# Kernel optimization log

Hardware: AMD Instinct MI355X
Metric: run time of the kernel (lower is better)

## Reference

```python
import jax, jax.numpy as jnp
import numpy as np

N_NODES = 50000
N_EDGES = 800000
IN_FEATS = 128
SAGE_HID = 512
H_FEATS = 128
MLP_HID = 32
N_PARTS = 8


def setup_inputs() -> dict:
    key = jax.random.key(0)
    ks = jax.random.split(key, 16)
    s = 0.05
    return {
        "features": jax.random.normal(ks[0], (N_NODES, IN_FEATS), jnp.float32),
        "src": jax.random.randint(ks[1], (N_EDGES,), 0, N_NODES),
        "dst": jax.random.randint(ks[2], (N_EDGES,), 0, N_NODES),
        # SAGEConv layer 1 (in_feats -> 512): fc_self has bias, fc_neigh no bias
        "W1_self": jax.random.normal(ks[3], (IN_FEATS, SAGE_HID), jnp.float32) * s,
        "W1_neigh": jax.random.normal(ks[4], (IN_FEATS, SAGE_HID), jnp.float32) * s,
        "b1": jnp.zeros((SAGE_HID,), jnp.float32),
        # SAGEConv layer 2 (512 -> h_feats)
        "W2_self": jax.random.normal(ks[5], (SAGE_HID, H_FEATS), jnp.float32) * s,
        "W2_neigh": jax.random.normal(ks[6], (SAGE_HID, H_FEATS), jnp.float32) * s,
        "b2": jnp.zeros((H_FEATS,), jnp.float32),
        # Partitioning MLP
        "Wp1": jax.random.normal(ks[7], (H_FEATS, MLP_HID), jnp.float32) * s,
        "bp1": jnp.zeros((MLP_HID,), jnp.float32),
        "Wp2": jax.random.normal(ks[8], (MLP_HID, N_PARTS), jnp.float32) * s,
        "bp2": jnp.zeros((N_PARTS,), jnp.float32),
    }


def _sage_mean(x, src, dst, deg_inv, W_self, W_neigh, b):
    # gather source-node features per edge, sum by destination, divide by in-degree
    agg = jax.ops.segment_sum(jnp.take(x, src, axis=0), dst, num_segments=N_NODES)
    agg = agg * deg_inv[:, None]
    return x @ W_self + agg @ W_neigh + b


def reference(features, src, dst, W1_self, W1_neigh, b1, W2_self, W2_neigh, b2,
              Wp1, bp1, Wp2, bp2):
    deg = jax.ops.segment_sum(jnp.ones_like(dst, dtype=features.dtype), dst,
                              num_segments=N_NODES)
    deg_inv = 1.0 / jnp.maximum(deg, 1.0)
    h = jax.nn.relu(_sage_mean(features, src, dst, deg_inv, W1_self, W1_neigh, b1))
    h = jax.nn.relu(_sage_mean(h, src, dst, deg_inv, W2_self, W2_neigh, b2))
    x = jax.nn.relu(h @ Wp1 + bp1)
    logits = x @ Wp2 + bp2
    return jax.nn.softmax(logits, axis=1)
```

## Files before the change

kernel.cpp:

```cpp
#include <hip/hip_runtime.h>
#include <hip/hip_bf16.h>

#define N_NODES 50000
#define N_EDGES 800000
#define ZROW    N_NODES
#define PADCAP  (N_EDGES + 8 * N_NODES + 64)
#define NCLS    8
#define CLSW    6250

typedef short  short8  __attribute__((ext_vector_type(8)));
typedef float  floatx4 __attribute__((ext_vector_type(4)));

__device__ __forceinline__ short f2bf(float f) {
    union { __hip_bfloat16 h; short s; } u;
    u.h = __float2bfloat16(f);
    return u.s;
}
__device__ __forceinline__ unsigned packbf(float lo, float hi) {
    return ((unsigned)(unsigned short)f2bf(hi) << 16) | (unsigned short)f2bf(lo);
}

__device__ __forceinline__ void acc2(unsigned v, float& ax, float& ay,
                                     unsigned selLo, unsigned selHi) {
    asm("v_dot2_f32_bf16 %0, %1, %2, %0" : "+v"(ax) : "v"(v), "v"(selLo));
    asm("v_dot2_f32_bf16 %0, %1, %2, %0" : "+v"(ay) : "v"(v), "v"(selHi));
}

__device__ __forceinline__ void gld_lds16(const short* g, short* l) {
    __builtin_amdgcn_global_load_lds(
        (const __attribute__((address_space(1))) int*)g,
        (__attribute__((address_space(3))) int*)l, 16, 0, 0);
}

__global__ void k_init(int* __restrict__ deg, int* __restrict__ col,
                       int* __restrict__ zrowA, int* __restrict__ zrowY) {
    int i = blockIdx.x * 256 + threadIdx.x;
    if (i < PADCAP) col[i] = ZROW;
    if (i < N_NODES) deg[i] = 0;
    if (i < 128) zrowA[i] = 0;
    if (i < 64)  zrowY[i] = 0;
}

__global__ void k_deg(const int* __restrict__ dst, int* __restrict__ deg) {
    int e = blockIdx.x * 256 + threadIdx.x;
    if (e < N_EDGES) atomicAdd(&deg[dst[e]], 1);
}

__global__ __launch_bounds__(1024) void k_scan1(const int* __restrict__ deg,
                                                int* __restrict__ bsum,
                                                float* __restrict__ dinv) {
    __shared__ int ws[16];
    int b = blockIdx.x, t = threadIdx.x, i = b * 1024 + t;
    int lane = t & 63, wid = t >> 6;
    int v = (i < N_NODES) ? deg[i] : 0;
    if (i < N_NODES) dinv[i] = 1.0f / fmaxf((float)v, 1.0f);
    int x = (v + 7) & ~7;
    #pragma unroll
    for (int off = 1; off < 64; off <<= 1) x += __shfl_xor(x, off, 64);
    if (lane == 0) ws[wid] = x;
    __syncthreads();
    if (t == 0) {
        int s = 0;
        #pragma unroll
        for (int k = 0; k < 16; ++k) s += ws[k];
        bsum[b] = s;
    }
}

__global__ void k_scan2(const int* __restrict__ bsum, int* __restrict__ boff) {
    int lane = threadIdx.x;
    int v = (lane < 49) ? bsum[lane] : 0;
    int x = v;
    #pragma unroll
    for (int off = 1; off < 64; off <<= 1) {
        int y = __shfl_up(x, off, 64);
        if (lane >= off) x += y;
    }
    if (lane < 49) boff[lane] = x - v;
}

__global__ __launch_bounds__(1024) void k_scan3(const int* __restrict__ deg,
                                                const int* __restrict__ boff,
                                                int* __restrict__ rowptr,
                                                int* __restrict__ cursor) {
    __shared__ int ws[16];
    int b = blockIdx.x, t = threadIdx.x, i = b * 1024 + t;
    int lane = t & 63, wid = t >> 6;
    int v = (i < N_NODES) ? ((deg[i] + 7) & ~7) : 0;
    int x = v;
    #pragma unroll
    for (int off = 1; off < 64; off <<= 1) {
        int y = __shfl_up(x, off, 64);
        if (lane >= off) x += y;
    }
    if (lane == 63) ws[wid] = x;
    __syncthreads();
    if (wid == 0) {
        int s = (lane < 16) ? ws[lane] : 0;
        #pragma unroll
        for (int off = 1; off < 16; off <<= 1) {
            int y = __shfl_up(s, off, 64);
            if (lane >= off) s += y;
        }
        if (lane < 16) ws[lane] = s;
    }
    __syncthreads();
    int waveOff = (wid == 0) ? 0 : ws[wid - 1];
    int incl = x + waveOff + boff[b];
    if (i < N_NODES) { rowptr[i + 1] = incl; cursor[i] = incl - v; }
    if (b == 0 && t == 0) rowptr[0] = 0;
}

__global__ __launch_bounds__(256) void k_fill(
    const int* __restrict__ src, const int* __restrict__ dst,
    int* __restrict__ cursor, int* __restrict__ col) {
    int b = blockIdx.x;
    int e = (b >> 3) * 256 + threadIdx.x;
    int lo = (b & 7) * CLSW;
    if (e < N_EDGES) {
        int d = dst[e];
        if ((unsigned)(d - lo) < CLSW) {
            int p = atomicAdd(&cursor[d], 1);
            col[p] = src[e];
        }
    }
}

__global__ void k_cvt(const float* __restrict__ feat,
                      const float* __restrict__ W1s, const float* __restrict__ W1n,
                      const float* __restrict__ W2s, const float* __restrict__ W2n,
                      const float* __restrict__ Wp1, const float* __restrict__ Wp2,
                      short* __restrict__ Abf, short* __restrict__ W1T,
                      short* __restrict__ W2T, float* __restrict__ Wp2T,
                      unsigned* __restrict__ W1pk) {
    int bb = blockIdx.x, t = threadIdx.x;
    if (bb < 6250) {
        int idx = bb * 256 + t;
        if (idx >= N_NODES * 32) return;
        int n = idx >> 5, c = (idx & 31) * 4;
        float4 v = *(const float4*)(feat + (size_t)n * 128 + c);
        *(short4*)(Abf + (size_t)n * 256 + c) =
            make_short4(f2bf(v.x), f2bf(v.y), f2bf(v.z), f2bf(v.w));
    } else {
        int idx = (bb - 6250) * 256 + t;
        if (idx < 512 * 256) {
            int n = idx >> 8, k = idx & 255;
            float v = (k < 128) ? W1s[(size_t)k * 512 + n]
                                : W1n[(size_t)(k - 128) * 512 + n];
            W1T[idx] = f2bf(v);
        } else if (idx < 2 * 512 * 256) {
            int j = idx - 512 * 256;
            int n = j >> 9, k = j & 511;
            float v = (n < 128) ? W2s[(size_t)k * 128 + n]
                                : W2n[(size_t)k * 128 + (n - 128)];
            W2T[j] = f2bf(v);
        } else {
            int r = idx - 2 * 512 * 256;
            if (r < 256) {
                Wp2T[r] = Wp2[(r & 31) * 8 + (r >> 5)];
            } else if (r < 256 + 2048) {
                int q = r - 256;
                int jj = q & 31, kp = (q >> 5) & 31, hh = q >> 10;
                int k0 = hh * 64 + 2 * kp;
                W1pk[q] = packbf(Wp1[(size_t)k0 * 32 + jj],
                                 Wp1[(size_t)(k0 + 1) * 32 + jj]);
            }
        }
    }
}

template<int STRIDE>
__device__ __forceinline__ float2 wave_gather(
    const unsigned* __restrict__ U, const int* __restrict__ col,
    int s, int e, int lane) {
    float ax = 0.f, ay = 0.f;
    unsigned selLo = 0x00003F80u;
    unsigned selHi = 0x3F800000u;
    for (int base = s; base < e; base += 64) {
        int cnt = e - base; if (cnt > 64) cnt = 64;
        int myc = col[base + lane];
        int j = 0;
        for (; j + 16 <= cnt; j += 16) {
            unsigned v[16];
            #pragma unroll
            for (int u = 0; u < 16; ++u) {
                int c = __builtin_amdgcn_readlane(myc, j + u);
                v[u] = U[(size_t)c * STRIDE + lane];
            }
            #pragma unroll
            for (int u = 0; u < 16; ++u) acc2(v[u], ax, ay, selLo, selHi);
        }
        for (; j < cnt; j += 8) {
            unsigned v[8];
            #pragma unroll
            for (int u = 0; u < 8; ++u) {
                int c = __builtin_amdgcn_readlane(myc, j + u);
                v[u] = U[(size_t)c * STRIDE + lane];
            }
            #pragma unroll
            for (int u = 0; u < 8; ++u) acc2(v[u], ax, ay, selLo, selHi);
        }
    }
    return make_float2(ax, ay);
}

__global__ __launch_bounds__(256) void k_agg(
    const unsigned* __restrict__ Au, const int* __restrict__ rowptr,
    const int* __restrict__ col, const float* __restrict__ dinv,
    unsigned* __restrict__ Aw) {
    int t = threadIdx.x, lane = t & 63, w = t >> 6;
    int n = blockIdx.x * 4 + w;
    int s = rowptr[n], e = rowptr[n + 1];
    float2 a = wave_gather<128>(Au, col, s, e, lane);
    float dv = dinv[n];
    Aw[(size_t)n * 128 + 64 + lane] = packbf(a.x * dv, a.y * dv);
}

__global__ __launch_bounds__(256) void k_aggmlp(
    const unsigned* __restrict__ Yu, const int* __restrict__ rowptr,
    const int* __restrict__ col, const float* __restrict__ dinv,
    const float* __restrict__ z, const float* __restrict__ b2,
    const unsigned* __restrict__ W1pk, const float* __restrict__ bp1,
    const float* __restrict__ Wp2T, const float* __restrict__ bp2,
    float* __restrict__ out) {
    __shared__ __align__(16) unsigned h2p[4][64];
    __shared__ __align__(16) float xsh[4][32];
    int t = threadIdx.x, lane = t & 63, w = t >> 6;
    int n = blockIdx.x * 4 + w;
    int s = rowptr[n], e = rowptr[n + 1];
    float2 a = wave_gather<64>(Yu, col, s, e, lane);
    float dv = dinv[n];
    float2 zv = *(const float2*)(z + (size_t)n * 128 + 2 * lane);
    float2 bb = *(const float2*)(b2 + 2 * lane);
    float h2x = fmaxf(zv.x + a.x * dv + bb.x, 0.f);
    float h2y = fmaxf(zv.y + a.y * dv + bb.y, 0.f);
    h2p[w][lane] = packbf(h2x, h2y);

    int j = lane & 31, half = lane >> 5;
    const unsigned* wp = W1pk + (half * 32) * 32 + j;
    float p = 0.f;
    #pragma unroll
    for (int kp = 0; kp < 32; ++kp) {
        unsigned hv = h2p[w][half * 32 + kp];
        unsigned wv = wp[kp * 32];
        asm("v_dot2_f32_bf16 %0, %1, %2, %0" : "+v"(p) : "v"(hv), "v"(wv));
    }
    p += __shfl_xor(p, 32, 64);
    if (half == 0) xsh[w][j] = fmaxf(p + bp1[j], 0.f);

    int j8 = lane >> 3, kg = lane & 7;
    float4 xv = *(const float4*)(&xsh[w][kg * 4]);
    float4 wv2 = *(const float4*)(Wp2T + j8 * 32 + kg * 4);
    float pp = xv.x * wv2.x + xv.y * wv2.y + xv.z * wv2.z + xv.w * wv2.w;
    pp += __shfl_xor(pp, 1, 64);
    pp += __shfl_xor(pp, 2, 64);
    pp += __shfl_xor(pp, 4, 64);
    float lg = pp + bp2[j8];
    float mx = lg;
    mx = fmaxf(mx, __shfl_xor(mx, 8, 64));
    mx = fmaxf(mx, __shfl_xor(mx, 16, 64));
    mx = fmaxf(mx, __shfl_xor(mx, 32, 64));
    float ev = expf(lg - mx);
    float sm = ev;
    sm += __shfl_xor(sm, 8, 64);
    sm += __shfl_xor(sm, 16, 64);
    sm += __shfl_xor(sm, 32, 64);
    if (kg == 0) out[(size_t)n * 8 + j8] = ev / sm;
}

template<int K, int N, bool EPI1>
__global__ __launch_bounds__(256) void k_gemm_mfma(
    const short* __restrict__ A, const short* __restrict__ BT,
    const float* __restrict__ bias, short* __restrict__ Obf,
    float* __restrict__ Of0) {
    __shared__ short smem[4 * 128 * 32];
    short* sOut = smem;
    const int t = threadIdx.x;
    const int lane = t & 63;
    const int w = t >> 6;
    const int mBase = blockIdx.x * 128;
    const int nBase = blockIdx.y * 128;
    const int mOff = (w & 1) * 64;
    const int nOff = (w >> 1) * 64;

    floatx4 zero4 = {0.f, 0.f, 0.f, 0.f};
    floatx4 acc[4][4];
    #pragma unroll
    for (int i = 0; i < 4; ++i)
        #pragma unroll
        for (int j = 0; j < 4; ++j) acc[i][j] = zero4;

    const int rL = lane >> 2;
    const int cg = (((lane & 3) ^ ((lane >> 3) & 3))) * 8;
    const int rA = w * 32 + rL;
    const long gA0 = (long)min(mBase + rA,      N_NODES - 1) * K + cg;
    const long gA1 = (long)min(mBase + rA + 16, N_NODES - 1) * K + cg;
    const long gB0 = (long)(nBase + rA)      * K + cg;
    const long gB1 = (long)(nBase + rA + 16) * K + cg;

    const int fr = lane & 15;
    const int csel = (((lane >> 4) ^ ((lane >> 1) & 3))) * 8;

    auto stage = [&](int b, int kt) {
        const int k0 = kt * 32;
        short* sA = smem + b * (2 * 128 * 32);
        short* sB = sA + 128 * 32;
        gld_lds16(A + gA0 + k0, sA + (w * 32) * 32);
        gld_lds16(A + gA1 + k0, sA + (w * 32 + 16) * 32);
        gld_lds16(BT + gB0 + k0, sB + (w * 32) * 32);
        gld_lds16(BT + gB1 + k0, sB + (w * 32 + 16) * 32);
    };

    stage(0, 0);
    int cur = 0;
    for (int kt = 0; kt < K / 32; ++kt) {
        __syncthreads();
        if (kt + 1 < K / 32) stage(cur ^ 1, kt + 1);
        const short* sA = smem + cur * (2 * 128 * 32);
        const short* sB = sA + 128 * 32;
        short8 af[4], bf[4];
        #pragma unroll
        for (int i = 0; i < 4; ++i) {
            af[i] = *(const short8*)(sA + (mOff + i * 16 + fr) * 32 + csel);
            bf[i] = *(const short8*)(sB + (nOff + i * 16 + fr) * 32 + csel);
        }
        #pragma unroll
        for (int mi = 0; mi < 4; ++mi)
            #pragma unroll
            for (int ni = 0; ni < 4; ++ni)
                acc[mi][ni] = __builtin_amdgcn_mfma_f32_16x16x32_bf16(
                    af[mi], bf[ni], acc[mi][ni], 0, 0, 0);
        cur ^= 1;
    }

    const int cn = lane & 15;
    const int cm = (lane >> 4) * 4;

    if (!EPI1 && nBase < 128) {
        #pragma unroll
        for (int ni = 0; ni < 4; ++ni) {
            const int n = nOff + ni * 16 + cn;
            #pragma unroll
            for (int mi = 0; mi < 4; ++mi) {
                #pragma unroll
                for (int r = 0; r < 4; ++r) {
                    const int m = mBase + mOff + mi * 16 + cm + r;
                    if (m < N_NODES) Of0[(size_t)m * 128 + n] = acc[mi][ni][r];
                }
            }
        }
        return;
    }

    float bv[4];
    #pragma unroll
    for (int ni = 0; ni < 4; ++ni)
        bv[ni] = EPI1 ? bias[nBase + nOff + ni * 16 + cn] : 0.f;
    const int myh = mOff >> 6;
    const int ldc = EPI1 ? N : 128;
    const int cbase = EPI1 ? nBase : 0;
    for (int h = 0; h < 2; ++h) {
        __syncthreads();
        if (myh == h) {
            #pragma unroll
            for (int mi = 0; mi < 4; ++mi)
                #pragma unroll
                for (int ni = 0; ni < 4; ++ni)
                    #pragma unroll
                    for (int r = 0; r < 4; ++r) {
                        int mrow = mi * 16 + cm + r;
                        int nloc = nOff + ni * 16 + cn;
                        float v = acc[mi][ni][r];
                        if (EPI1) v = fmaxf(v + bv[ni], 0.f);
                        sOut[mrow * 128 + nloc] = f2bf(v);
                    }
        }
        __syncthreads();
        int r0 = t >> 2, c0 = (t & 3) * 32;
        int m = mBase + h * 64 + r0;
        if (m < N_NODES) {
            const short* sp = sOut + r0 * 128 + c0;
            short* gp = Obf + (size_t)m * ldc + cbase + c0;
            #pragma unroll
            for (int q = 0; q < 4; ++q)
                *(short8*)(gp + q * 8) = *(const short8*)(sp + q * 8);
        }
    }
}

extern "C" void kernel_launch(void* const* d_in, const int* in_sizes, int n_in,
                              void* d_out, int out_size, void* d_ws, size_t ws_size,
                              hipStream_t stream) {
    const float* feat   = (const float*)d_in[0];
    const int*   src    = (const int*)d_in[1];
    const int*   dst    = (const int*)d_in[2];
    const float* W1s    = (const float*)d_in[3];
    const float* W1n    = (const float*)d_in[4];
    const float* b1     = (const float*)d_in[5];
    const float* W2s    = (const float*)d_in[6];
    const float* W2n    = (const float*)d_in[7];
    const float* b2     = (const float*)d_in[8];
    const float* Wp1    = (const float*)d_in[9];
    const float* bp1    = (const float*)d_in[10];
    const float* Wp2    = (const float*)d_in[11];
    const float* bp2    = (const float*)d_in[12];
    float* out = (float*)d_out;

    char* w = (char*)d_ws;
    size_t off = 0;
    auto alloc = [&](size_t bytes) { char* p = w + off; off += (bytes + 255) & ~(size_t)255; return p; };
    int*   deg    = (int*)alloc(N_NODES * 4);
    int*   rowptr = (int*)alloc((N_NODES + 1) * 4);
    int*   cursor = (int*)alloc(N_NODES * 4);
    int*   col    = (int*)alloc((size_t)PADCAP * 4);
    float* dinv   = (float*)alloc(N_NODES * 4);
    int*   bsum   = (int*)alloc(64 * 4);
    int*   boff   = (int*)alloc(64 * 4);
    short* Abf    = (short*)alloc((size_t)(N_NODES + 1) * 256 * 2);
    short* W1T    = (short*)alloc((size_t)512 * 256 * 2);
    short* W2T    = (short*)alloc((size_t)256 * 512 * 2);
    short* h1bf   = (short*)alloc((size_t)N_NODES * 512 * 2);
    float* z      = (float*)alloc((size_t)N_NODES * 128 * 4);
    short* y1bf   = (short*)alloc((size_t)(N_NODES + 1) * 128 * 2);
    float* Wp2T   = (float*)alloc((size_t)8 * 32 * 4);
    unsigned* W1pk = (unsigned*)alloc((size_t)2048 * 4);

    k_init<<<(PADCAP + 255) / 256, 256, 0, stream>>>(
        deg, col, (int*)(Abf + (size_t)N_NODES * 256),
        (int*)(y1bf + (size_t)N_NODES * 128));
    k_deg<<<N_EDGES / 256, 256, 0, stream>>>(dst, deg);
    k_scan1<<<49, 1024, 0, stream>>>(deg, bsum, dinv);
    k_scan2<<<1, 64, 0, stream>>>(bsum, boff);
    k_scan3<<<49, 1024, 0, stream>>>(deg, boff, rowptr, cursor);
    k_fill<<<NCLS * (N_EDGES / 256), 256, 0, stream>>>(src, dst, cursor, col);
    k_cvt<<<7283, 256, 0, stream>>>(feat, W1s, W1n, W2s, W2n, Wp1, Wp2,
                                    Abf, W1T, W2T, Wp2T, W1pk);
    k_agg<<<N_NODES / 4, 256, 0, stream>>>((const unsigned*)Abf, rowptr, col, dinv, (unsigned*)Abf);
    dim3 g1((N_NODES + 127) / 128, 4);
    k_gemm_mfma<256, 512, true><<<g1, 256, 0, stream>>>(Abf, W1T, b1, h1bf, nullptr);
    dim3 g2((N_NODES + 127) / 128, 2);
    k_gemm_mfma<512, 256, false><<<g2, 256, 0, stream>>>(h1bf, W2T, nullptr, y1bf, z);
    k_aggmlp<<<N_NODES / 4, 256, 0, stream>>>((const unsigned*)y1bf, rowptr, col, dinv, z, b2,
                                              W1pk, bp1, Wp2T, bp2, out);
}
```

Before: 310.7 us.

## Fuse the two SAGE GEMMs into one kernel keeping the hidden tile in LDS

Replaces the two separate MFMA GEMM launches with a single kernel that computes a 64-row tile of the 512-wide hidden layer, applies bias and ReLU, keeps it in shared memory, and immediately multiplies it by the second-layer weights to produce z and y1. This removes the global write and re-read of the 50000x512 bf16 hidden activation and one launch. In exchange, each block streams both full weight matrices, uses a smaller 64-row tile, and needs about 115 KB of dynamic LDS, which limits occupancy.

```diff
diff --git a/kernel.cpp b/kernel.cpp
--- a/kernel.cpp
+++ b/kernel.cpp
@@ -7,6 +7,7 @@
 #define PADCAP  (N_EDGES + 8 * N_NODES + 64)
 #define NCLS    8
 #define CLSW    6250
+#define FUSED_LDS_BYTES ((16384 + 8192 + 64 * 520) * 2)
 
 typedef short  short8  __attribute__((ext_vector_type(8)));
 typedef float  floatx4 __attribute__((ext_vector_type(4)));
@@ -268,122 +269,163 @@
     if (kg == 0) out[(size_t)n * 8 + j8] = ev / sm;
 }
 
-template<int K, int N, bool EPI1>
-__global__ __launch_bounds__(256) void k_gemm_mfma(
-    const short* __restrict__ A, const short* __restrict__ BT,
-    const float* __restrict__ bias, short* __restrict__ Obf,
-    float* __restrict__ Of0) {
-    __shared__ short smem[4 * 128 * 32];
-    short* sOut = smem;
+__global__ __launch_bounds__(256) void k_gemm12(
+    const short* __restrict__ A, const short* __restrict__ W1T,
+    const float* __restrict__ b1, const short* __restrict__ W2T,
+    float* __restrict__ z, short* __restrict__ y1bf) {
+    extern __shared__ short smem[];
+    short* A_lds  = smem;
+    short* wstage = smem + 16384;
+    short* h1     = smem + 24576;
+    short* sOut   = wstage;
+
     const int t = threadIdx.x;
     const int lane = t & 63;
     const int w = t >> 6;
-    const int mBase = blockIdx.x * 128;
-    const int nBase = blockIdx.y * 128;
-    const int mOff = (w & 1) * 64;
-    const int nOff = (w >> 1) * 64;
-
-    floatx4 zero4 = {0.f, 0.f, 0.f, 0.f};
-    floatx4 acc[4][4];
-    #pragma unroll
-    for (int i = 0; i < 4; ++i)
-        #pragma unroll
-        for (int j = 0; j < 4; ++j) acc[i][j] = zero4;
+    const int mBase = blockIdx.x * 64;
 
     const int rL = lane >> 2;
     const int cg = (((lane & 3) ^ ((lane >> 3) & 3))) * 8;
-    const int rA = w * 32 + rL;
-    const long gA0 = (long)min(mBase + rA,      N_NODES - 1) * K + cg;
-    const long gA1 = (long)min(mBase + rA + 16, N_NODES - 1) * K + cg;
-    const long gB0 = (long)(nBase + rA)      * K + cg;
-    const long gB1 = (long)(nBase + rA + 16) * K + cg;
-
     const int fr = lane & 15;
     const int csel = (((lane >> 4) ^ ((lane >> 1) & 3))) * 8;
-
-    auto stage = [&](int b, int kt) {
-        const int k0 = kt * 32;
-        short* sA = smem + b * (2 * 128 * 32);
-        short* sB = sA + 128 * 32;
-        gld_lds16(A + gA0 + k0, sA + (w * 32) * 32);
-        gld_lds16(A + gA1 + k0, sA + (w * 32 + 16) * 32);
-        gld_lds16(BT + gB0 + k0, sB + (w * 32) * 32);
-        gld_lds16(BT + gB1 + k0, sB + (w * 32 + 16) * 32);
-    };
-
-    stage(0, 0);
-    int cur = 0;
-    for (int kt = 0; kt < K / 32; ++kt) {
-        __syncthreads();
-        if (kt + 1 < K / 32) stage(cur ^ 1, kt + 1);
-        const short* sA = smem + cur * (2 * 128 * 32);
-        const short* sB = sA + 128 * 32;
-        short8 af[4], bf[4];
-        #pragma unroll
-        for (int i = 0; i < 4; ++i) {
-            af[i] = *(const short8*)(sA + (mOff + i * 16 + fr) * 32 + csel);
-            bf[i] = *(const short8*)(sB + (nOff + i * 16 + fr) * 32 + csel);
-        }
-        #pragma unroll
-        for (int mi = 0; mi < 4; ++mi)
-            #pragma unroll
-            for (int ni = 0; ni < 4; ++ni)
-                acc[mi][ni] = __builtin_amdgcn_mfma_f32_16x16x32_bf16(
-                    af[mi], bf[ni], acc[mi][ni], 0, 0, 0);
-        cur ^= 1;
-    }
-
+    const int q8 = (lane >> 4) * 8;
+    const int mOff = (w & 1) * 32;
+    const int nOff = (w >> 1) * 64;
     const int cn = lane & 15;
     const int cm = (lane >> 4) * 4;
 
-    if (!EPI1 && nBase < 128) {
+    {
+        const long ar = (long)min(mBase + w * 16 + rL, N_NODES - 1) * 256 + cg;
         #pragma unroll
-        for (int ni = 0; ni < 4; ++ni) {
-            const int n = nOff + ni * 16 + cn;
-            #pragma unroll
-            for (int mi = 0; mi < 4; ++mi) {
-                #pragma unroll
-                for (int r = 0; r < 4; ++r) {
-                    const int m = mBase + mOff + mi * 16 + cm + r;
-                    if (m < N_NODES) Of0[(size_t)m * 128 + n] = acc[mi][ni][r];
+        for (int kt = 0; kt < 8; ++kt)
+            gld_lds16(A + ar + kt * 32, A_lds + kt * 2048 + (w * 16) * 32);
+    }
+
+    floatx4 zero4 = {0.f, 0.f, 0.f, 0.f};
+    floatx4 acc[2][4];
+
+    {
+        const long r0base = (long)(w * 32 + rL) * 256 + cg;
+        auto stage1 = [&](int b, int step) {
+            int nc = step >> 3, kt = step & 7;
+            const long r0 = r0base + (long)nc * (128 * 256) + kt * 32;
+            short* d = wstage + b * 4096 + (w * 32) * 32;
+            gld_lds16(W1T + r0,            d);
+            gld_lds16(W1T + r0 + 16 * 256, d + 16 * 32);
+        };
+        stage1(0, 0);
+        int cur = 0;
+        for (int nc = 0; nc < 4; ++nc) {
+            #pragma unroll
+            for (int mi = 0; mi < 2; ++mi)
+                #pragma unroll
+                for (int ni = 0; ni < 4; ++ni) acc[mi][ni] = zero4;
+            for (int kt = 0; kt < 8; ++kt) {
+                int step = nc * 8 + kt;
+                __syncthreads();
+                if (step + 1 < 32) stage1(cur ^ 1, step + 1);
+                const short* sB = wstage + cur * 4096;
+                short8 af[2], bf[4];
+                #pragma unroll
+                for (int i = 0; i < 2; ++i)
+                    af[i] = *(const short8*)(A_lds + kt * 2048 +
+                                             (mOff + i * 16 + fr) * 32 + csel);
+                #pragma unroll
+                for (int i = 0; i < 4; ++i)
+                    bf[i] = *(const short8*)(sB + (nOff + i * 16 + fr) * 32 + csel);
+                #pragma unroll
+                for (int mi = 0; mi < 2; ++mi)
+                    #pragma unroll
+                    for (int ni = 0; ni < 4; ++ni)
+                        acc[mi][ni] = __builtin_amdgcn_mfma_f32_16x16x32_bf16(
+                            af[mi], bf[ni], acc[mi][ni], 0, 0, 0);
+                cur ^= 1;
+            }
+            #pragma unroll
+            for (int ni = 0; ni < 4; ++ni) {
+                int colc = nc * 128 + nOff + ni * 16 + cn;
+                float bv = b1[colc];
+                #pragma unroll
+                for (int mi = 0; mi < 2; ++mi)
+                    #pragma unroll
+                    for (int r = 0; r < 4; ++r)
+                        h1[(mOff + mi * 16 + cm + r) * 520 + colc] =
+                            f2bf(fmaxf(acc[mi][ni][r] + bv, 0.f));
+            }
+        }
+    }
+    __syncthreads();
+
+    {
+        const long r0base = (long)(w * 32 + rL) * 512 + cg;
+        auto stage2 = [&](int b, int step) {
+            int nc = step >> 4, kt = step & 15;
+            const long r0 = r0base + (long)nc * (128 * 512) + kt * 32;
+            short* d = wstage + b * 4096 + (w * 32) * 32;
+            gld_lds16(W2T + r0,            d);
+            gld_lds16(W2T + r0 + 16 * 512, d + 16 * 32);
+        };
+        stage2(0, 0);
+        int cur = 0;
+        for (int nc2 = 0; nc2 < 2; ++nc2) {
+            #pragma unroll
+            for (int mi = 0; mi < 2; ++mi)
+                #pragma unroll
+                for (int ni = 0; ni < 4; ++ni) acc[mi][ni] = zero4;
+            for (int kt = 0; kt < 16; ++kt) {
+                int step = nc2 * 16 + kt;
+                __syncthreads();
+                if (step + 1 < 32) stage2(cur ^ 1, step + 1);
+                const short* sB = wstage + cur * 4096;
+                short8 af[2], bf[4];
+                #pragma unroll
+                for (int i = 0; i < 2; ++i)
+                    af[i] = *(const short8*)(h1 + (mOff + i * 16 + fr) * 520 +
+                                             kt * 32 + q8);
+                #pragma unroll
+                for (int i = 0; i < 4; ++i)
+                    bf[i] = *(const short8*)(sB + (nOff + i * 16 + fr) * 32 + csel);
+                #pragma unroll
+                for (int mi = 0; mi < 2; ++mi)
+                    #pragma unroll
+                    for (int ni = 0; ni < 4; ++ni)
+                        acc[mi][ni] = __builtin_amdgcn_mfma_f32_16x16x32_bf16(
+                            af[mi], bf[ni], acc[mi][ni], 0, 0, 0);
+                cur ^= 1;
+            }
+            if (nc2 == 0) {
+                #pragma unroll
+                for (int ni = 0; ni < 4; ++ni) {
+                    int n = nOff + ni * 16 + cn;
+                    #pragma unroll
+                    for (int mi = 0; mi < 2; ++mi)
+                        #pragma unroll
+                        for (int r = 0; r < 4; ++r) {
+                            int m = mBase + mOff + mi * 16 + cm + r;
+                            if (m < N_NODES) z[(size_t)m * 128 + n] = acc[mi][ni][r];
+                        }
                 }
-            }
-        }
-        return;
-    }
-
-    float bv[4];
-    #pragma unroll
-    for (int ni = 0; ni < 4; ++ni)
-        bv[ni] = EPI1 ? bias[nBase + nOff + ni * 16 + cn] : 0.f;
-    const int myh = mOff >> 6;
-    const int ldc = EPI1 ? N : 128;
-    const int cbase = EPI1 ? nBase : 0;
-    for (int h = 0; h < 2; ++h) {
-        __syncthreads();
-        if (myh == h) {
-            #pragma unroll
-            for (int mi = 0; mi < 4; ++mi)
+            } else {
+                __syncthreads();
                 #pragma unroll
                 for (int ni = 0; ni < 4; ++ni)
                     #pragma unroll
-                    for (int r = 0; r < 4; ++r) {
-                        int mrow = mi * 16 + cm + r;
-                        int nloc = nOff + ni * 16 + cn;
-                        float v = acc[mi][ni][r];
-                        if (EPI1) v = fmaxf(v + bv[ni], 0.f);
-                        sOut[mrow * 128 + nloc] = f2bf(v);
-                    }
-        }
-        __syncthreads();
-        int r0 = t >> 2, c0 = (t & 3) * 32;
-        int m = mBase + h * 64 + r0;
-        if (m < N_NODES) {
-            const short* sp = sOut + r0 * 128 + c0;
-            short* gp = Obf + (size_t)m * ldc + cbase + c0;
-            #pragma unroll
-            for (int q = 0; q < 4; ++q)
-                *(short8*)(gp + q * 8) = *(const short8*)(sp + q * 8);
+                    for (int mi = 0; mi < 2; ++mi)
+                        #pragma unroll
+                        for (int r = 0; r < 4; ++r)
+                            sOut[(mOff + mi * 16 + cm + r) * 128 +
+                                 nOff + ni * 16 + cn] = f2bf(acc[mi][ni][r]);
+                __syncthreads();
+                int r0 = t >> 2, c0 = (t & 3) * 32;
+                int m = mBase + r0;
+                if (m < N_NODES) {
+                    const short* sp = sOut + r0 * 128 + c0;
+                    short* gp = y1bf + (size_t)m * 128 + c0;
+                    #pragma unroll
+                    for (int qq = 0; qq < 4; ++qq)
+                        *(short8*)(gp + qq * 8) = *(const short8*)(sp + qq * 8);
+                }
+            }
         }
     }
 }
@@ -419,11 +461,18 @@
     short* Abf    = (short*)alloc((size_t)(N_NODES + 1) * 256 * 2);
     short* W1T    = (short*)alloc((size_t)512 * 256 * 2);
     short* W2T    = (short*)alloc((size_t)256 * 512 * 2);
-    short* h1bf   = (short*)alloc((size_t)N_NODES * 512 * 2);
     float* z      = (float*)alloc((size_t)N_NODES * 128 * 4);
     short* y1bf   = (short*)alloc((size_t)(N_NODES + 1) * 128 * 2);
     float* Wp2T   = (float*)alloc((size_t)8 * 32 * 4);
     unsigned* W1pk = (unsigned*)alloc((size_t)2048 * 4);
+
+    static bool attrSet = false;
+    if (!attrSet) {
+        hipFuncSetAttribute((const void*)k_gemm12,
+                            hipFuncAttributeMaxDynamicSharedMemorySize,
+                            FUSED_LDS_BYTES);
+        attrSet = true;
+    }
 
     k_init<<<(PADCAP + 255) / 256, 256, 0, stream>>>(
         deg, col, (int*)(Abf + (size_t)N_NODES * 256),
@@ -436,10 +485,8 @@
     k_cvt<<<7283, 256, 0, stream>>>(feat, W1s, W1n, W2s, W2n, Wp1, Wp2,
                                     Abf, W1T, W2T, Wp2T, W1pk);
     k_agg<<<N_NODES / 4, 256, 0, stream>>>((const unsigned*)Abf, rowptr, col, dinv, (unsigned*)Abf);
-    dim3 g1((N_NODES + 127) / 128, 4);
-    k_gemm_mfma<256, 512, true><<<g1, 256, 0, stream>>>(Abf, W1T, b1, h1bf, nullptr);
-    dim3 g2((N_NODES + 127) / 128, 2);
-    k_gemm_mfma<512, 256, false><<<g2, 256, 0, stream>>>(h1bf, W2T, nullptr, y1bf, z);
+    k_gemm12<<<(N_NODES + 63) / 64, 256, FUSED_LDS_BYTES, stream>>>(
+        Abf, W1T, b1, W2T, z, y1bf);
     k_aggmlp<<<N_NODES / 4, 256, 0, stream>>>((const unsigned*)y1bf, rowptr, col, dinv, z, b2,
                                               W1pk, bp1, Wp2T, bp2, out);
 }
```

Result: slower. 324.4 us (+4.4%).
